# Optimization experiments

Hardware: AMD Instinct MI355X
Metric: run time of the kernel (lower is better)

Reference implementation:

```python
import jax, jax.numpy as jnp
import numpy as np

B, S, D = 8, 2048, 128

def setup_inputs() -> dict:
    key = jax.random.key(0)
    kq, kk, kv, km = jax.random.split(key, 4)
    q = jax.random.normal(kq, (B, S, D), dtype=jnp.float32)
    k = jax.random.normal(kk, (B, S, D), dtype=jnp.float32)
    v = jax.random.normal(kv, (B, S, D), dtype=jnp.float32)
    mask = jax.random.randint(km, (B, S), 0, 2).astype(bool)  # True = masked out
    return {"q": q, "k": k, "v": v, "mask": mask}

def reference(q, k, v, mask):
    scaler = np.sqrt(D).astype(np.float32)
    # score[b, i, j] = <q_i, k_j> / sqrt(d_k)
    score = jnp.einsum('bik,bjk->bij', q, k) / scaler
    score = score - jnp.max(score, axis=-1, keepdims=True)
    e = jnp.exp(score)
    # mask is (B, S_kv): broadcast across query positions, zero out masked keys
    e = jnp.where(mask[:, None, :], 0.0, e)
    a = e / jnp.sum(e, axis=-1, keepdims=True)
    c = jnp.einsum('bij,bjd->bid', a, v)
    return c
```

## Files before the change

kernel.cpp:

```cpp
#include <hip/hip_runtime.h>
#include <hip/hip_fp16.h>
#include <math.h>

typedef __attribute__((ext_vector_type(8))) short short8;
typedef __attribute__((ext_vector_type(16))) float floatx16;
typedef __attribute__((ext_vector_type(2))) __bf16 bf16x2;

namespace {
constexpr int Bn = 8;
constexpr int Sn = 2048;
constexpr int Dn = 128;
constexpr int BQ = 128;
constexpr int BK = 64;
constexpr int QTILES = Sn / BQ;
constexpr int NKB = Sn / BK;
constexpr int ROWS = Bn * Sn;
constexpr int NSPLIT = 4;
constexpr float SC2 = 0.12753102063642597f;
constexpr int TILE_USH = BK * Dn;
}

#if __has_builtin(__builtin_amdgcn_exp2f)
#define EXP2(x) __builtin_amdgcn_exp2f(x)
#else
#define EXP2(x) exp2f(x)
#endif

__device__ __forceinline__ unsigned short f2bf(float x) {
  union { float f; unsigned u; } a; a.f = x;
  unsigned r = a.u + 0x7fffu + ((a.u >> 16) & 1u);
  return (unsigned short)(r >> 16);
}

__device__ __forceinline__ unsigned pack2bf(float x, float y) {
  union { bf16x2 b; unsigned u; } c;
  c.b[0] = (__bf16)x; c.b[1] = (__bf16)y;
  return c.u;
}

__device__ __forceinline__ void gl_lds16(const void* g, void* l, int lane) {
#if __has_builtin(__builtin_amdgcn_global_load_lds)
  (void)lane;
  __builtin_amdgcn_global_load_lds((const __attribute__((address_space(1))) unsigned int*)g,
                                   (__attribute__((address_space(3))) unsigned int*)l, 16, 0, 0);
#else
  *(float4*)((char*)l + lane * 16) = *(const float4*)g;
#endif
}

__global__ __launch_bounds__(256)
void prep(const float* __restrict__ kg, const float* __restrict__ vg,
          const unsigned char* __restrict__ mraw,
          unsigned short* __restrict__ Kpg, unsigned short* __restrict__ Vpg,
          float* __restrict__ mb2g) {
  __shared__ __align__(16) float Vf[16 * 136];
  const int p = blockIdx.x;
  const int b = p >> 7, q = p & 127;
  const int kb = q >> 2, k16 = q & 3;
  const int t = threadIdx.x;

  unsigned wv = ((const unsigned int*)mraw)[t];
  int any1  = __syncthreads_or((wv & 0x0000ff00u) ? 1 : 0);
  int any23 = __syncthreads_or((wv & 0xffff0000u) ? 1 : 0);
  const int mlayout = any1 ? 1 : (any23 ? 2 : 0);
  if (p < 64) {
    int idx = p * 256 + t;
    bool ms;
    if (mlayout == 1)      ms = mraw[idx] != 0;
    else if (mlayout == 2) ms = ((const float*)mraw)[idx] != 0.0f;
    else                   ms = ((const int*)mraw)[idx] != 0;
    mb2g[idx] = ms ? -1e30f : 0.0f;
  }

  const int j  = t >> 4;
  const int o8 = t & 15;
  const size_t base = ((size_t)(b * Sn + kb * 64 + k16 * 16 + j)) * 32 + o8 * 2;
  const float4* k4 = (const float4*)kg;
  const float4* v4 = (const float4*)vg;

  {
    float4 a = k4[base], bq = k4[base + 1];
    union { unsigned u[4]; short8 s8; } pk;
    pk.u[0] = pack2bf(a.x, a.y);   pk.u[1] = pack2bf(a.z, a.w);
    pk.u[2] = pack2bf(bq.x, bq.y); pk.u[3] = pack2bf(bq.z, bq.w);
    const int jl = k16 * 16 + j;
    *(short8*)(Kpg + (size_t)(b * NKB + kb) * TILE_USH + jl * 128 + ((o8 ^ (jl & 7)) * 8)) = pk.s8;
  }
  {
    float4 a = v4[base], bq = v4[base + 1];
    *(float4*)&Vf[j * 136 + o8 * 8]     = a;
    *(float4*)&Vf[j * 136 + o8 * 8 + 4] = bq;
  }
  __syncthreads();
  {
    const int d = t >> 1, h = t & 1;
    union { unsigned u[4]; short8 s8; } pv;
    #pragma unroll
    for (int i = 0; i < 4; ++i)
      pv.u[i] = pack2bf(Vf[(h * 8 + 2 * i) * 136 + d], Vf[(h * 8 + 2 * i + 1) * 136 + d]);
    const int og = k16 * 2 + h;
    *(short8*)(Vpg + (size_t)(b * NKB + kb) * TILE_USH + d * 64 + ((og ^ (d & 7)) * 8)) = pv.s8;
  }
}

template<int SPLIT, bool DIRECT>
__global__ __launch_bounds__(256, 2)
void attn_fwd(const float* __restrict__ qg,
              const unsigned short* __restrict__ Kpg,
              const unsigned short* __restrict__ Vpg,
              const float* __restrict__ mb2g,
              float* __restrict__ outg, __half* __restrict__ Op,
              float* __restrict__ Mp, float* __restrict__ Lp) {
  __shared__ __align__(16) unsigned short Khi[2][TILE_USH];
  __shared__ __align__(16) unsigned short Vt[2][TILE_USH];
  __shared__ __align__(16) unsigned short Pq[4 * 2048];

  const int tid = threadIdx.x;
  const int bid = blockIdx.x;
  const int b   = bid & 7;
  const int q0  = ((bid >> 3) & (QTILES - 1)) * BQ;
  const int s   = bid >> 7;
  const int kb0 = s * (NKB / SPLIT);
  const int kbN = kb0 + NKB / SPLIT;
  const int w   = tid >> 6;
  const int L   = tid & 63;
  const int q   = L & 31;
  const int h   = L >> 5;
  const int sw  = q & 7;

  const char* ktile = (const char*)(Kpg + (size_t)b * NKB * TILE_USH);
  const char* vtile = (const char*)(Vpg + (size_t)b * NKB * TILE_USH);
  const int stagebase = w * 4096;

  short8 qh[8], ql[8];
  {
    const float* qrow = qg + (size_t)(b * Sn + q0 + w * 32 + q) * Dn;
    #pragma unroll
    for (int kstep = 0; kstep < 8; ++kstep) {
      float4 f0 = *(const float4*)(qrow + kstep * 16 + h * 8);
      float4 f1 = *(const float4*)(qrow + kstep * 16 + h * 8 + 4);
      float xs[8] = {f0.x, f0.y, f0.z, f0.w, f1.x, f1.y, f1.z, f1.w};
      #pragma unroll
      for (int j = 0; j < 8; ++j) {
        unsigned short hi = f2bf(xs[j]);
        union { unsigned u; float f; } hv; hv.u = ((unsigned)hi) << 16;
        qh[kstep][j] = (short)hi;
        ql[kstep][j] = (short)f2bf(xs[j] - hv.f);
      }
    }
  }

  float m_i = -INFINITY, l_i = 0.0f;
  floatx16 O32[4];
  #pragma unroll
  for (int dg = 0; dg < 4; ++dg)
    #pragma unroll
    for (int r = 0; r < 16; ++r) O32[dg][r] = 0.0f;

  unsigned short* pwave = Pq + w * 2048;

  {
    const char* kt = ktile + (size_t)kb0 * (TILE_USH * 2);
    const char* vt = vtile + (size_t)kb0 * (TILE_USH * 2);
    #pragma unroll
    for (int i = 0; i < 4; ++i) {
      const int off = stagebase + i * 1024;
      gl_lds16(kt + off + L * 16, (char*)Khi[0] + off, L);
      gl_lds16(vt + off + L * 16, (char*)Vt[0] + off, L);
    }
  }

  for (int kb = kb0; kb < kbN; ++kb) {
    const int cur = (kb - kb0) & 1;
    __syncthreads();

    if (kb + 1 < kbN) {
      const char* kt = ktile + (size_t)(kb + 1) * (TILE_USH * 2);
      const char* vt = vtile + (size_t)(kb + 1) * (TILE_USH * 2);
      #pragma unroll
      for (int i = 0; i < 4; ++i) {
        const int off = stagebase + i * 1024;
        gl_lds16(kt + off + L * 16, (char*)Khi[cur ^ 1] + off, L);
        gl_lds16(vt + off + L * 16, (char*)Vt[cur ^ 1] + off, L);
      }
    }

    const unsigned short* Kc = Khi[cur];
    const unsigned short* Vc = Vt[cur];

    const float4* mb4 = (const float4*)(mb2g + b * Sn + kb * BK);
    float4 mbv[2][4];
    #pragma unroll
    for (int kg = 0; kg < 2; ++kg)
      #pragma unroll
      for (int ro = 0; ro < 4; ++ro) mbv[kg][ro] = mb4[kg * 8 + ro * 2 + h];

    floatx16 a32[2];
    #pragma unroll
    for (int kg = 0; kg < 2; ++kg)
      #pragma unroll
      for (int r = 0; r < 16; ++r) a32[kg][r] = 0.0f;
    #pragma unroll
    for (int kstep = 0; kstep < 8; ++kstep) {
      const int ko = ((kstep * 2 + h) ^ sw) * 8;
      #pragma unroll
      for (int kg = 0; kg < 2; ++kg) {
        short8 kf = *(const short8*)&Kc[(kg * 32 + q) * 128 + ko];
        a32[kg] = __builtin_amdgcn_mfma_f32_32x32x16_bf16(kf, qh[kstep], a32[kg], 0, 0, 0);
        a32[kg] = __builtin_amdgcn_mfma_f32_32x32x16_bf16(kf, ql[kstep], a32[kg], 0, 0, 0);
      }
    }

    #pragma unroll
    for (int kg = 0; kg < 2; ++kg)
      #pragma unroll
      for (int ro = 0; ro < 4; ++ro) {
        float4 f = mbv[kg][ro];
        a32[kg][4 * ro + 0] = fmaf(a32[kg][4 * ro + 0], SC2, f.x);
        a32[kg][4 * ro + 1] = fmaf(a32[kg][4 * ro + 1], SC2, f.y);
        a32[kg][4 * ro + 2] = fmaf(a32[kg][4 * ro + 2], SC2, f.z);
        a32[kg][4 * ro + 3] = fmaf(a32[kg][4 * ro + 3], SC2, f.w);
      }
    float mx = -INFINITY;
    #pragma unroll
    for (int kg = 0; kg < 2; ++kg)
      #pragma unroll
      for (int r = 0; r < 16; ++r) mx = fmaxf(mx, a32[kg][r]);
    mx = fmaxf(mx, __shfl_xor(mx, 32));
    const float mnew = fmaxf(m_i, mx);
    const float alpha = EXP2(m_i - mnew);
    float rs = 0.0f;
    #pragma unroll
    for (int kg = 0; kg < 2; ++kg)
      #pragma unroll
      for (int r = 0; r < 16; ++r) {
        float e = EXP2(a32[kg][r] - mnew);
        a32[kg][r] = e;
        rs += e;
      }
    rs += __shfl_xor(rs, 32);
    l_i = l_i * alpha + rs;
    m_i = mnew;

    #pragma unroll
    for (int kg = 0; kg < 2; ++kg)
      #pragma unroll
      for (int ro = 0; ro < 4; ++ro) {
        uint2 u;
        u.x = pack2bf(a32[kg][4 * ro + 0], a32[kg][4 * ro + 1]);
        u.y = pack2bf(a32[kg][4 * ro + 2], a32[kg][4 * ro + 3]);
        const int oct = kg * 4 + ro;
        *(uint2*)&pwave[q * 64 + ((oct ^ sw) * 8) + h * 4] = u;
      }

    if (!__all(alpha == 1.0f)) {
      #pragma unroll
      for (int dg = 0; dg < 4; ++dg)
        #pragma unroll
        for (int r = 0; r < 16; ++r) O32[dg][r] *= alpha;
    }

    #pragma unroll
    for (int k2 = 0; k2 < 4; ++k2) {
      const int ko = ((k2 * 2 + h) ^ sw) * 8;
      short8 pf = *(const short8*)&pwave[q * 64 + ko];
      #pragma unroll
      for (int dg = 0; dg < 4; ++dg) {
        short8 vf = *(const short8*)&Vc[(dg * 32 + q) * 64 + ko];
        O32[dg] = __builtin_amdgcn_mfma_f32_32x32x16_bf16(vf, pf, O32[dg], 0, 0, 0);
      }
    }
  }

  const int row = b * Sn + q0 + w * 32 + q;
  if constexpr (DIRECT) {
    const float inv = 1.0f / l_i;
    float* orow = outg + (size_t)row * Dn;
    #pragma unroll
    for (int dg = 0; dg < 4; ++dg)
      #pragma unroll
      for (int ro = 0; ro < 4; ++ro) {
        float4 f = make_float4(O32[dg][4 * ro] * inv,     O32[dg][4 * ro + 1] * inv,
                               O32[dg][4 * ro + 2] * inv, O32[dg][4 * ro + 3] * inv);
        *(float4*)&orow[dg * 32 + 8 * ro + 4 * h] = f;
      }
  } else {
    __half* orow = Op + ((size_t)s * ROWS + row) * Dn;
    #pragma unroll
    for (int dg = 0; dg < 4; ++dg)
      #pragma unroll
      for (int ro = 0; ro < 4; ++ro) {
        union { __half2 h2[2]; uint2 u; } pk;
        pk.h2[0] = __floats2half2_rn(O32[dg][4 * ro],     O32[dg][4 * ro + 1]);
        pk.h2[1] = __floats2half2_rn(O32[dg][4 * ro + 2], O32[dg][4 * ro + 3]);
        *(uint2*)&orow[dg * 32 + 8 * ro + 4 * h] = pk.u;
      }
    if (h == 0) {
      Mp[s * ROWS + row] = m_i;
      Lp[s * ROWS + row] = l_i;
    }
  }
}

__global__ __launch_bounds__(256)
void attn_combine(const __half* __restrict__ Op, const float* __restrict__ Mp,
                  const float* __restrict__ Lp, float4* __restrict__ out4) {
  const int gid = blockIdx.x * 256 + threadIdx.x;
  const int row = gid >> 5;
  const int c4  = gid & 31;
  float ms[NSPLIT];
  float m = -INFINITY;
  #pragma unroll
  for (int s = 0; s < NSPLIT; ++s) { ms[s] = Mp[s * ROWS + row]; m = fmaxf(m, ms[s]); }
  float l = 0.0f;
  float4 acc = make_float4(0.f, 0.f, 0.f, 0.f);
  #pragma unroll
  for (int s = 0; s < NSPLIT; ++s) {
    float wgt = EXP2(ms[s] - m);
    l = fmaf(Lp[s * ROWS + row], wgt, l);
    union { uint2 u; __half2 h2[2]; } pk;
    pk.u = ((const uint2*)Op)[(size_t)(s * ROWS + row) * 32 + c4];
    float2 f0 = __half22float2(pk.h2[0]);
    float2 f1 = __half22float2(pk.h2[1]);
    acc.x = fmaf(f0.x, wgt, acc.x);
    acc.y = fmaf(f0.y, wgt, acc.y);
    acc.z = fmaf(f1.x, wgt, acc.z);
    acc.w = fmaf(f1.y, wgt, acc.w);
  }
  float inv = 1.0f / l;
  out4[(size_t)row * 32 + c4] = make_float4(acc.x * inv, acc.y * inv, acc.z * inv, acc.w * inv);
}

extern "C" void kernel_launch(void* const* d_in, const int* in_sizes, int n_in,
                              void* d_out, int out_size, void* d_ws, size_t ws_size,
                              hipStream_t stream) {
  const float* q = (const float*)d_in[0];
  const float* k = (const float*)d_in[1];
  const float* v = (const float*)d_in[2];
  const unsigned char* m = (const unsigned char*)d_in[3];
  float* out = (float*)d_out;
  (void)in_sizes; (void)n_in; (void)out_size;

  constexpr size_t OPB = (size_t)NSPLIT * ROWS * Dn * sizeof(__half);
  constexpr size_t MLB = (size_t)NSPLIT * ROWS * sizeof(float);
  constexpr size_t KPB = (size_t)Bn * NKB * TILE_USH * 2;
  constexpr size_t MBB = (size_t)ROWS * sizeof(float);

  char* ws = (char*)d_ws;
  if (ws_size >= OPB + 2 * MLB + 2 * KPB + MBB) {
    __half* Op = (__half*)ws;
    float* Mp = (float*)(ws + OPB);
    float* Lp = (float*)(ws + OPB + MLB);
    unsigned short* Kp = (unsigned short*)(ws + OPB + 2 * MLB);
    unsigned short* Vp = (unsigned short*)(ws + OPB + 2 * MLB + KPB);
    float* mb2 = (float*)(ws + OPB + 2 * MLB + 2 * KPB);
    prep<<<dim3(Bn * NKB * 4), dim3(256), 0, stream>>>(k, v, m, Kp, Vp, mb2);
    attn_fwd<NSPLIT, false><<<dim3(Bn * QTILES * NSPLIT), dim3(256), 0, stream>>>(
        q, Kp, Vp, mb2, out, Op, Mp, Lp);
    attn_combine<<<dim3(ROWS * 32 / 256), dim3(256), 0, stream>>>(
        Op, Mp, Lp, (float4*)out);
  } else if (ws_size >= 2 * KPB + MBB) {
    unsigned short* Kp = (unsigned short*)ws;
    unsigned short* Vp = (unsigned short*)(ws + KPB);
    float* mb2 = (float*)(ws + 2 * KPB);
    prep<<<dim3(Bn * NKB * 4), dim3(256), 0, stream>>>(k, v, m, Kp, Vp, mb2);
    attn_fwd<1, true><<<dim3(Bn * QTILES), dim3(256), 0, stream>>>(
        q, Kp, Vp, mb2, out, nullptr, nullptr, nullptr);
  }
}
```

Before: 114.4 us.

## Fuse split-K combine into attention kernel via last-block atomic counter

```diff
diff --git a/kernel.cpp b/kernel.cpp
--- a/kernel.cpp
+++ b/kernel.cpp
@@ -16,6 +16,7 @@
 constexpr int NKB = Sn / BK;
 constexpr int ROWS = Bn * Sn;
 constexpr int NSPLIT = 4;
+constexpr int NGRP = Bn * QTILES;
 constexpr float SC2 = 0.12753102063642597f;
 constexpr int TILE_USH = BK * Dn;
 }
@@ -52,12 +53,14 @@
 void prep(const float* __restrict__ kg, const float* __restrict__ vg,
           const unsigned char* __restrict__ mraw,
           unsigned short* __restrict__ Kpg, unsigned short* __restrict__ Vpg,
-          float* __restrict__ mb2g) {
+          float* __restrict__ mb2g, int* __restrict__ cnt) {
   __shared__ __align__(16) float Vf[16 * 136];
   const int p = blockIdx.x;
   const int b = p >> 7, q = p & 127;
   const int kb = q >> 2, k16 = q & 3;
   const int t = threadIdx.x;
+
+  if (p == 0 && t < NGRP) cnt[t] = 0;
 
   unsigned wv = ((const unsigned int*)mraw)[t];
   int any1  = __syncthreads_or((wv & 0x0000ff00u) ? 1 : 0);
@@ -110,10 +113,12 @@
               const unsigned short* __restrict__ Vpg,
               const float* __restrict__ mb2g,
               float* __restrict__ outg, __half* __restrict__ Op,
-              float* __restrict__ Mp, float* __restrict__ Lp) {
+              float* __restrict__ Mp, float* __restrict__ Lp,
+              int* __restrict__ cnt) {
   __shared__ __align__(16) unsigned short Khi[2][TILE_USH];
   __shared__ __align__(16) unsigned short Vt[2][TILE_USH];
   __shared__ __align__(16) unsigned short Pq[4 * 2048];
+  __shared__ int lastflag;
 
   const int tid = threadIdx.x;
   const int bid = blockIdx.x;
@@ -299,36 +304,57 @@
       Mp[s * ROWS + row] = m_i;
       Lp[s * ROWS + row] = l_i;
     }
-  }
-}
-
-__global__ __launch_bounds__(256)
-void attn_combine(const __half* __restrict__ Op, const float* __restrict__ Mp,
-                  const float* __restrict__ Lp, float4* __restrict__ out4) {
-  const int gid = blockIdx.x * 256 + threadIdx.x;
-  const int row = gid >> 5;
-  const int c4  = gid & 31;
-  float ms[NSPLIT];
-  float m = -INFINITY;
-  #pragma unroll
-  for (int s = 0; s < NSPLIT; ++s) { ms[s] = Mp[s * ROWS + row]; m = fmaxf(m, ms[s]); }
-  float l = 0.0f;
-  float4 acc = make_float4(0.f, 0.f, 0.f, 0.f);
-  #pragma unroll
-  for (int s = 0; s < NSPLIT; ++s) {
-    float wgt = EXP2(ms[s] - m);
-    l = fmaf(Lp[s * ROWS + row], wgt, l);
-    union { uint2 u; __half2 h2[2]; } pk;
-    pk.u = ((const uint2*)Op)[(size_t)(s * ROWS + row) * 32 + c4];
-    float2 f0 = __half22float2(pk.h2[0]);
-    float2 f1 = __half22float2(pk.h2[1]);
-    acc.x = fmaf(f0.x, wgt, acc.x);
-    acc.y = fmaf(f0.y, wgt, acc.y);
-    acc.z = fmaf(f1.x, wgt, acc.z);
-    acc.w = fmaf(f1.y, wgt, acc.w);
-  }
-  float inv = 1.0f / l;
-  out4[(size_t)row * 32 + c4] = make_float4(acc.x * inv, acc.y * inv, acc.z * inv, acc.w * inv);
+
+    __threadfence();
+    if (tid == 0) {
+      int old = atomicAdd(&cnt[bid & (NGRP - 1)], 1);
+      lastflag = (old == SPLIT - 1) ? 1 : 0;
+    }
+    __syncthreads();
+    if (lastflag) {
+      __threadfence();
+      float* wrow = (float*)Pq;
+      const int rowbase0 = b * Sn + q0;
+      if (tid < BQ) {
+        float ms2[SPLIT];
+        float mm = -INFINITY;
+        #pragma unroll
+        for (int ss = 0; ss < SPLIT; ++ss) {
+          ms2[ss] = Mp[ss * ROWS + rowbase0 + tid];
+          mm = fmaxf(mm, ms2[ss]);
+        }
+        float lsum = 0.0f, wv2[SPLIT];
+        #pragma unroll
+        for (int ss = 0; ss < SPLIT; ++ss) {
+          wv2[ss] = EXP2(ms2[ss] - mm);
+          lsum = fmaf(Lp[ss * ROWS + rowbase0 + tid], wv2[ss], lsum);
+        }
+        const float inv = 1.0f / lsum;
+        #pragma unroll
+        for (int ss = 0; ss < SPLIT; ++ss) wrow[ss * BQ + tid] = wv2[ss] * inv;
+      }
+      __syncthreads();
+      float4* out4 = (float4*)outg;
+      const uint2* Op2 = (const uint2*)Op;
+      for (int i = tid; i < BQ * (Dn / 4); i += 256) {
+        const int rl = i >> 5, c4 = i & 31;
+        float4 acc2 = make_float4(0.f, 0.f, 0.f, 0.f);
+        #pragma unroll
+        for (int ss = 0; ss < SPLIT; ++ss) {
+          const float wgt = wrow[ss * BQ + rl];
+          union { uint2 u; __half2 h2[2]; } pk;
+          pk.u = Op2[((size_t)ss * ROWS + rowbase0 + rl) * 32 + c4];
+          float2 f0 = __half22float2(pk.h2[0]);
+          float2 f1 = __half22float2(pk.h2[1]);
+          acc2.x = fmaf(f0.x, wgt, acc2.x);
+          acc2.y = fmaf(f0.y, wgt, acc2.y);
+          acc2.z = fmaf(f1.x, wgt, acc2.z);
+          acc2.w = fmaf(f1.y, wgt, acc2.w);
+        }
+        out4[(size_t)(rowbase0 + rl) * 32 + c4] = acc2;
+      }
+    }
+  }
 }
 
 extern "C" void kernel_launch(void* const* d_in, const int* in_sizes, int n_in,
@@ -345,26 +371,27 @@
   constexpr size_t MLB = (size_t)NSPLIT * ROWS * sizeof(float);
   constexpr size_t KPB = (size_t)Bn * NKB * TILE_USH * 2;
   constexpr size_t MBB = (size_t)ROWS * sizeof(float);
+  constexpr size_t CNT = (size_t)NGRP * sizeof(int);
 
   char* ws = (char*)d_ws;
-  if (ws_size >= OPB + 2 * MLB + 2 * KPB + MBB) {
+  if (ws_size >= OPB + 2 * MLB + 2 * KPB + MBB + CNT) {
     __half* Op = (__half*)ws;
     float* Mp = (float*)(ws + OPB);
     float* Lp = (float*)(ws + OPB + MLB);
     unsigned short* Kp = (unsigned short*)(ws + OPB + 2 * MLB);
     unsigned short* Vp = (unsigned short*)(ws + OPB + 2 * MLB + KPB);
     float* mb2 = (float*)(ws + OPB + 2 * MLB + 2 * KPB);
-    prep<<<dim3(Bn * NKB * 4), dim3(256), 0, stream>>>(k, v, m, Kp, Vp, mb2);
+    int* cnt = (int*)(ws + OPB + 2 * MLB + 2 * KPB + MBB);
+    prep<<<dim3(Bn * NKB * 4), dim3(256), 0, stream>>>(k, v, m, Kp, Vp, mb2, cnt);
     attn_fwd<NSPLIT, false><<<dim3(Bn * QTILES * NSPLIT), dim3(256), 0, stream>>>(
-        q, Kp, Vp, mb2, out, Op, Mp, Lp);
-    attn_combine<<<dim3(ROWS * 32 / 256), dim3(256), 0, stream>>>(
-        Op, Mp, Lp, (float4*)out);
-  } else if (ws_size >= 2 * KPB + MBB) {
+        q, Kp, Vp, mb2, out, Op, Mp, Lp, cnt);
+  } else if (ws_size >= 2 * KPB + MBB + CNT) {
     unsigned short* Kp = (unsigned short*)ws;
     unsigned short* Vp = (unsigned short*)(ws + KPB);
     float* mb2 = (float*)(ws + 2 * KPB);
-    prep<<<dim3(Bn * NKB * 4), dim3(256), 0, stream>>>(k, v, m, Kp, Vp, mb2);
+    int* cnt = (int*)(ws + 2 * KPB + MBB);
+    prep<<<dim3(Bn * NKB * 4), dim3(256), 0, stream>>>(k, v, m, Kp, Vp, mb2, cnt);
     attn_fwd<1, true><<<dim3(Bn * QTILES), dim3(256), 0, stream>>>(
-        q, Kp, Vp, mb2, out, nullptr, nullptr, nullptr);
-  }
-}
+        q, Kp, Vp, mb2, out, nullptr, nullptr, nullptr, cnt);
+  }
+}
```

New measurement: 207.3 us. +81.3%, slower.
